# Performance work log

Hardware: AMD Instinct MI355X
Metric: run time of the kernel (lower is better)

The kernel has to match this reference:

```python
import jax, jax.numpy as jnp
import numpy as np

BETA = 0.1       # reputation weight
GAMMA = 0.1      # load penalty weight
EXPL_C = 0.1     # UCB exploration constant
LOAD_EMA = 0.9   # load EMA alpha
TOP_K = 2
EPS = 1e-10


def setup_inputs() -> dict:
    key = jax.random.key(0)
    k1, k2, k3, k4, k5 = jax.random.split(key, 5)
    B, S, H, E = 4, 4096, 2048, 64
    return {
        "x": jax.random.normal(k1, (B, S, H), dtype=jnp.float32),
        "gate_w": jax.random.normal(k2, (E, H), dtype=jnp.float32) * (1.0 / np.sqrt(H)),
        "reputation": jax.random.normal(k3, (E,), dtype=jnp.float32),
        "loads": jax.random.uniform(k4, (E,), dtype=jnp.float32),
        "counts": jax.random.uniform(k5, (E,), dtype=jnp.float32),
        "total_decisions": 1000000,
    }


def reference(x, gate_w, reputation, loads, counts, total_decisions):
    B, S, H = x.shape
    E = gate_w.shape[0]
    x_flat = x.reshape(-1, H)                                  # [T, H]
    base_logits = jnp.einsum("th,eh->te", x_flat, gate_w)      # [T, E]

    # current_batch_assignments is None -> current_loads = expert_loads
    updated_loads = LOAD_EMA * loads + (1.0 - LOAD_EMA) * loads  # [E]

    # UCB-style exploration bonus, broadcast over tokens
    expl = EXPL_C * jnp.sqrt(jnp.log(jnp.float32(total_decisions) + 1.0) / (counts + EPS))  # [E]

    selection_scores = (base_logits
                        + BETA * reputation[None, :]
                        - GAMMA * updated_loads[None, :]
                        + expl[None, :])                        # [T, E]

    top_k_scores, top_k_indices = jax.lax.top_k(selection_scores, TOP_K)  # [T, K]
    routing_weights = jax.nn.softmax(top_k_scores, axis=-1).reshape(B, S, TOP_K)
    expert_indices = top_k_indices.reshape(B, S, TOP_K)

    # differentiable load-balancing aux loss
    router_probs = jax.nn.softmax(selection_scores.astype(jnp.float32), axis=-1)  # [T, E]
    expert_gate = jax.nn.one_hot(top_k_indices, E, dtype=jnp.float32).sum(axis=1)  # [T, E]
    tokens_per_expert = expert_gate.mean(axis=0)               # [E]
    router_prob_per_expert = router_probs.mean(axis=0)         # [E]
    aux_loss = (tokens_per_expert * router_prob_per_expert).sum() * E

    return routing_weights, expert_indices, aux_loss
```

## Files before the change

kernel.cpp:

```cpp
#include <hip/hip_runtime.h>
#include <cmath>

#define HDIM 2048
#define H4   (HDIM / 4)
#define NEXP 64
#define TTOT 16384
#define KSPLIT 2
#define KBLK (HDIM / KSPLIT)
#define BKC  64
#define NCHUNK (KBLK / BKC)
#define BTOK 64
#define LDT  72
#define LDS_SC 65

#define WS_PARTIAL_OFF 128
#define PARTIAL_FLOATS ((size_t)(TTOT / BTOK) * KSPLIT * BTOK * NEXP)

typedef short  bf16x8 __attribute__((ext_vector_type(8)));
typedef float  f32x16 __attribute__((ext_vector_type(16)));

__device__ __forceinline__ unsigned bf_rn_u(float f, float* back) {
    unsigned u = __float_as_uint(f);
    unsigned r = (u + 0x7fffu + ((u >> 16) & 1u)) & 0xffff0000u;
    *back = __uint_as_float(r);
    return r;
}

__global__ __launch_bounds__(256, 2) void router_gemm_mfma(
    const float* __restrict__ x,
    const float* __restrict__ gw,
    float* __restrict__ partial,
    float* __restrict__ accs)
{
    __shared__ short aT[3][BTOK][LDT];
    __shared__ short bT[3][NEXP][LDT];

    const int tid  = threadIdx.x;
    const int lane = tid & 63;
    const int l31  = lane & 31;
    const int lhi  = lane >> 5;
    const int w    = tid >> 6;
    const int wm   = w & 1;
    const int wn   = w >> 1;
    const int tb   = blockIdx.x;
    const int kg   = blockIdx.y;
    const int T0   = tb * BTOK;

    if (tb == 0 && kg == 0 && tid < 2 * NEXP) accs[tid] = 0.0f;

    const int srow = tid >> 2;
    const int scol = tid & 3;

    const float4* __restrict__ x4 = reinterpret_cast<const float4*>(x)
        + (size_t)(T0 + srow) * H4 + (size_t)kg * (H4 / 2) + scol;
    const float4* __restrict__ g4 = reinterpret_cast<const float4*>(gw)
        + (size_t)srow * H4 + (size_t)kg * (H4 / 2) + scol;

    f32x16 acc;
    #pragma unroll
    for (int i = 0; i < 16; ++i) acc[i] = 0.0f;

    const short* aP[3];
    const short* bP[3];
    #pragma unroll
    for (int v = 0; v < 3; ++v) {
        aP[v] = &aT[v][32 * wm + l31][8 * lhi];
        bP[v] = &bT[v][32 * wn + l31][8 * lhi];
    }

    float4 xa[4], xb[4];

#define LOAD_CHUNK(CH) do {                                                    \
        _Pragma("unroll")                                                      \
        for (int j = 0; j < 4; ++j) {                                          \
            xa[j] = x4[(CH) * (BKC / 4) + 4 * j];                              \
            xb[j] = g4[(CH) * (BKC / 4) + 4 * j];                              \
        } } while (0)

#define SPLIT_STORE(TILE, ROW, FV, JJ) do {                                    \
        const float _f[4] = {(FV).x, (FV).y, (FV).z, (FV).w};                  \
        unsigned _h[4], _m[4], _l[4];                                          \
        _Pragma("unroll")                                                      \
        for (int u = 0; u < 4; ++u) {                                          \
            float _b0, _b1;                                                    \
            _h[u] = bf_rn_u(_f[u], &_b0);                                      \
            const float _r1 = _f[u] - _b0;                                     \
            _m[u] = bf_rn_u(_r1, &_b1);                                        \
            const float _r2 = _r1 - _b1;                                       \
            _l[u] = __float_as_uint(_r2) + 0x8000u;                            \
        }                                                                      \
        const int _kl = 4 * (scol + 4 * (JJ));                                 \
        *reinterpret_cast<uint2*>(&TILE[0][ROW][_kl]) =                        \
            make_uint2(__builtin_amdgcn_perm(_h[1], _h[0], 0x07060302u),       \
                       __builtin_amdgcn_perm(_h[3], _h[2], 0x07060302u));      \
        *reinterpret_cast<uint2*>(&TILE[1][ROW][_kl]) =                        \
            make_uint2(__builtin_amdgcn_perm(_m[1], _m[0], 0x07060302u),       \
                       __builtin_amdgcn_perm(_m[3], _m[2], 0x07060302u));      \
        *reinterpret_cast<uint2*>(&TILE[2][ROW][_kl]) =                        \
            make_uint2(__builtin_amdgcn_perm(_l[1], _l[0], 0x07060302u),       \
                       __builtin_amdgcn_perm(_l[3], _l[2], 0x07060302u));      \
    } while (0)

    LOAD_CHUNK(0);

    for (int ch = 0; ch < NCHUNK; ++ch) {
        #pragma unroll
        for (int j = 0; j < 4; ++j) {
            SPLIT_STORE(aT, srow, xa[j], j);
            SPLIT_STORE(bT, srow, xb[j], j);
        }
        __syncthreads();

        if (ch + 1 < NCHUNK) LOAD_CHUNK(ch + 1);

        #pragma unroll
        for (int ks = 0; ks < 4; ++ks) {
            bf16x8 ah = *reinterpret_cast<const bf16x8*>(aP[0] + 16 * ks);
            bf16x8 am = *reinterpret_cast<const bf16x8*>(aP[1] + 16 * ks);
            bf16x8 al = *reinterpret_cast<const bf16x8*>(aP[2] + 16 * ks);
            bf16x8 bh = *reinterpret_cast<const bf16x8*>(bP[0] + 16 * ks);
            bf16x8 bm = *reinterpret_cast<const bf16x8*>(bP[1] + 16 * ks);
            bf16x8 bl = *reinterpret_cast<const bf16x8*>(bP[2] + 16 * ks);
            acc = __builtin_amdgcn_mfma_f32_32x32x16_bf16(ah, bh, acc, 0, 0, 0);
            acc = __builtin_amdgcn_mfma_f32_32x32x16_bf16(ah, bm, acc, 0, 0, 0);
            acc = __builtin_amdgcn_mfma_f32_32x32x16_bf16(am, bh, acc, 0, 0, 0);
            acc = __builtin_amdgcn_mfma_f32_32x32x16_bf16(ah, bl, acc, 0, 0, 0);
            acc = __builtin_amdgcn_mfma_f32_32x32x16_bf16(am, bm, acc, 0, 0, 0);
            acc = __builtin_amdgcn_mfma_f32_32x32x16_bf16(al, bh, acc, 0, 0, 0);
        }
        __syncthreads();
    }
#undef LOAD_CHUNK
#undef SPLIT_STORE

    float* pbase = partial + ((size_t)tb * KSPLIT + kg) * (BTOK * NEXP);
    const int e = 32 * wn + l31;
    #pragma unroll
    for (int r = 0; r < 16; ++r) {
        const int t_loc = 32 * wm + (r & 3) + 8 * (r >> 2) + 4 * lhi;
        pbase[(size_t)t_loc * NEXP + e] = acc[r];
    }
}

__global__ __launch_bounds__(256) void router_reduce(
    const float* __restrict__ partial,
    const float* __restrict__ rep,
    const float* __restrict__ loads,
    const float* __restrict__ counts,
    const int*   __restrict__ total_dec,
    float* __restrict__ out_w,
    float* __restrict__ out_idx,
    float* __restrict__ prob_acc,
    float* __restrict__ gate_acc)
{
    __shared__ float sc_s[BTOK][LDS_SC];
    __shared__ float bias_s[NEXP];
    __shared__ float m_s[BTOK], zi_s[BTOK];
    __shared__ int   i1_s[BTOK], i2_s[BTOK];

    const int tid = threadIdx.x;
    const int rt  = blockIdx.x;
    const int t0  = rt * BTOK;

    if (tid < NEXP) {
        float L = logf((float)(*total_dec) + 1.0f);
        bias_s[tid] = 0.1f * rep[tid] - 0.1f * loads[tid]
                    + 0.1f * sqrtf(L / (counts[tid] + 1e-10f));
    }
    __syncthreads();

    const float* p = partial + (size_t)rt * KSPLIT * (BTOK * NEXP);
    #pragma unroll
    for (int o = 0; o < (BTOK * NEXP) / 256; ++o) {
        const int idx = o * 256 + tid;
        float s = p[idx] + p[BTOK * NEXP + idx];
        sc_s[idx >> 6][idx & 63] = s + bias_s[idx & 63];
    }
    __syncthreads();

    if (tid < BTOK) {
        const int t = tid;
        float m1 = -INFINITY, m2 = -INFINITY;
        int   i1 = 0, i2 = 0;
        for (int e = 0; e < NEXP; ++e) {
            const float s = sc_s[t][e];
            if (s > m1)      { m2 = m1; i2 = i1; m1 = s; i1 = e; }
            else if (s > m2) { m2 = s; i2 = e; }
        }
        float z = 0.0f;
        for (int e = 0; e < NEXP; ++e) z += __expf(sc_s[t][e] - m1);

        const float e2  = expf(m2 - m1);
        const float inv = 1.0f / (1.0f + e2);
        const int   gt  = t0 + t;
        reinterpret_cast<float2*>(out_w)[gt]   = make_float2(inv, e2 * inv);
        reinterpret_cast<float2*>(out_idx)[gt] = make_float2((float)i1, (float)i2);
        m_s[t] = m1; zi_s[t] = 1.0f / z; i1_s[t] = i1; i2_s[t] = i2;
    }
    __syncthreads();

    if (tid < NEXP) {
        const int e = tid;
        float ps = 0.0f, gs = 0.0f;
        for (int t = 0; t < BTOK; ++t) {
            ps += __expf(sc_s[t][e] - m_s[t]) * zi_s[t];
            gs += (float)((i1_s[t] == e) + (i2_s[t] == e));
        }
        atomicAdd(&prob_acc[e], ps);
        atomicAdd(&gate_acc[e], gs);
    }
}

#define BKF  32
#define LDAF (64 + 4)
__global__ __launch_bounds__(256) void router_main(
    const float* __restrict__ x,
    const float* __restrict__ gw,
    const float* __restrict__ rep,
    const float* __restrict__ loads,
    const float* __restrict__ counts,
    const int*   __restrict__ total_dec,
    float* __restrict__ out_w,
    float* __restrict__ out_idx,
    float* __restrict__ prob_acc,
    float* __restrict__ gate_acc)
{
    __shared__ float a_s[2][BKF][LDAF];
    __shared__ float b_s[2][BKF][LDAF];
    __shared__ float sc_s[64][LDS_SC];
    __shared__ float bias_s[NEXP];
    __shared__ float m_s[64], z_s[64];
    __shared__ int   i1_s[64], i2_s[64];

    const int tid = threadIdx.x;
    const int tx  = tid & 15;
    const int ty  = tid >> 4;
    const int r0  = tid >> 3;
    const int c4  = tid & 7;
    const int t0  = blockIdx.x * 64;

    if (tid < NEXP) {
        float L = logf((float)(*total_dec) + 1.0f);
        bias_s[tid] = 0.1f * rep[tid] - 0.1f * loads[tid]
                    + 0.1f * sqrtf(L / (counts[tid] + 1e-10f));
    }

    const float4* __restrict__ x4 = reinterpret_cast<const float4*>(x) + (size_t)t0 * H4;
    const float4* __restrict__ g4 = reinterpret_cast<const float4*>(gw);

    float acc[4][4] = {};

#define STORE_TILE(BUFI, A0, A1, B0, B1) do {                                  \
        float _t0[4] = {(A0).x, (A0).y, (A0).z, (A0).w};                       \
        float _t1[4] = {(A1).x, (A1).y, (A1).z, (A1).w};                       \
        float _t2[4] = {(B0).x, (B0).y, (B0).z, (B0).w};                       \
        float _t3[4] = {(B1).x, (B1).y, (B1).z, (B1).w};                       \
        _Pragma("unroll")                                                      \
        for (int u = 0; u < 4; ++u) {                                          \
            a_s[BUFI][c4 * 4 + u][r0]      = _t0[u];                           \
            a_s[BUFI][c4 * 4 + u][r0 + 32] = _t1[u];                           \
            b_s[BUFI][c4 * 4 + u][r0]      = _t2[u];                           \
            b_s[BUFI][c4 * 4 + u][r0 + 32] = _t3[u];                           \
        } } while (0)

    {
        float4 a0 = x4[(size_t)r0 * H4 + c4];
        float4 a1 = x4[(size_t)(r0 + 32) * H4 + c4];
        float4 b0 = g4[(size_t)r0 * H4 + c4];
        float4 b1 = g4[(size_t)(r0 + 32) * H4 + c4];
        STORE_TILE(0, a0, a1, b0, b1);
    }
    __syncthreads();

    int buf = 0;
    for (int it = 0; it < HDIM / BKF; ++it) {
        float4 na0, na1, nb0, nb1;
        const bool has_next = (it + 1 < HDIM / BKF);
        if (has_next) {
            const int k4 = (it + 1) * (BKF / 4);
            na0 = x4[(size_t)r0 * H4 + k4 + c4];
            na1 = x4[(size_t)(r0 + 32) * H4 + k4 + c4];
            nb0 = g4[(size_t)r0 * H4 + k4 + c4];
            nb1 = g4[(size_t)(r0 + 32) * H4 + k4 + c4];
        }
        #pragma unroll
        for (int kk = 0; kk < BKF; ++kk) {
            const float4 afv = *reinterpret_cast<const float4*>(&a_s[buf][kk][ty * 4]);
            const float4 bfv = *reinterpret_cast<const float4*>(&b_s[buf][kk][tx * 4]);
            const float af[4] = {afv.x, afv.y, afv.z, afv.w};
            const float bf[4] = {bfv.x, bfv.y, bfv.z, bfv.w};
            #pragma unroll
            for (int i = 0; i < 4; ++i)
                #pragma unroll
                for (int j = 0; j < 4; ++j)
                    acc[i][j] = fmaf(af[i], bf[j], acc[i][j]);
        }
        if (has_next) STORE_TILE(buf ^ 1, na0, na1, nb0, nb1);
        __syncthreads();
        buf ^= 1;
    }
#undef STORE_TILE

    #pragma unroll
    for (int i = 0; i < 4; ++i)
        #pragma unroll
        for (int j = 0; j < 4; ++j)
            sc_s[ty * 4 + i][tx * 4 + j] = acc[i][j] + bias_s[tx * 4 + j];
    __syncthreads();

    if (tid < 64) {
        const int t = tid;
        float m1 = -INFINITY, m2 = -INFINITY;
        int   i1 = 0, i2 = 0;
        for (int e = 0; e < NEXP; ++e) {
            const float s = sc_s[t][e];
            if (s > m1)      { m2 = m1; i2 = i1; m1 = s; i1 = e; }
            else if (s > m2) { m2 = s; i2 = e; }
        }
        float z = 0.0f;
        for (int e = 0; e < NEXP; ++e) z += expf(sc_s[t][e] - m1);
        const float e2  = expf(m2 - m1);
        const float inv = 1.0f / (1.0f + e2);
        const int   gt  = t0 + t;
        reinterpret_cast<float2*>(out_w)[gt]   = make_float2(inv, e2 * inv);
        reinterpret_cast<float2*>(out_idx)[gt] = make_float2((float)i1, (float)i2);
        m_s[t] = m1; z_s[t] = z; i1_s[t] = i1; i2_s[t] = i2;
    }
    __syncthreads();

    if (tid < NEXP) {
        const int e = tid;
        float ps = 0.0f, gs = 0.0f;
        for (int t = 0; t < 64; ++t) {
            ps += expf(sc_s[t][e] - m_s[t]) / z_s[t];
            gs += (float)((i1_s[t] == e) + (i2_s[t] == e));
        }
        atomicAdd(&prob_acc[e], ps);
        atomicAdd(&gate_acc[e], gs);
    }
}

__global__ void router_aux(const float* __restrict__ prob_acc,
                           const float* __restrict__ gate_acc,
                           float* __restrict__ out_aux)
{
    const float invT = 1.0f / (float)TTOT;
    const int e = threadIdx.x;
    float v = (gate_acc[e] * invT) * (prob_acc[e] * invT);
    #pragma unroll
    for (int off = 32; off > 0; off >>= 1)
        v += __shfl_down(v, off);
    if (e == 0) out_aux[0] = v * (float)NEXP;
}

extern "C" void kernel_launch(void* const* d_in, const int* in_sizes, int n_in,
                              void* d_out, int out_size, void* d_ws, size_t ws_size,
                              hipStream_t stream)
{
    const float* x      = (const float*)d_in[0];
    const float* gw     = (const float*)d_in[1];
    const float* rep    = (const float*)d_in[2];
    const float* loads  = (const float*)d_in[3];
    const float* counts = (const float*)d_in[4];
    const int*   total  = (const int*)d_in[5];

    float* out     = (float*)d_out;
    float* out_w   = out;
    float* out_idx = out + 32768;
    float* out_aux = out + 65536;

    float* prob_acc = (float*)d_ws;
    float* gate_acc = prob_acc + NEXP;
    float* partial  = (float*)d_ws + WS_PARTIAL_OFF;

    const size_t ws_needed = (WS_PARTIAL_OFF + PARTIAL_FLOATS) * sizeof(float);

    if (ws_size >= ws_needed) {
        router_gemm_mfma<<<dim3(TTOT / BTOK, KSPLIT), dim3(256), 0, stream>>>(
            x, gw, partial, prob_acc);
        router_reduce<<<dim3(TTOT / BTOK), dim3(256), 0, stream>>>(
            partial, rep, loads, counts, total, out_w, out_idx, prob_acc, gate_acc);
    } else {
        hipMemsetAsync(d_ws, 0, WS_PARTIAL_OFF * sizeof(float), stream);
        router_main<<<dim3(TTOT / 64), dim3(256), 0, stream>>>(
            x, gw, rep, loads, counts, total, out_w, out_idx, prob_acc, gate_acc);
    }
    router_aux<<<dim3(1), dim3(64), 0, stream>>>(prob_acc, gate_acc, out_aux);
}
```

Baseline: 228.9 us.

## Pre-split gate weights into bf16x3 once and stream them into the GEMM

Adds a small kernel that splits gate_w into three bf16 planes (hi/mid/lo) in workspace once per call, so the 256x2 GEMM blocks load the pre-split weights instead of each redoing the fp32 to bf16x3 split. The per-element split on both operands is also rewritten to use packed hardware bf16 conversion. This removes redundant VALU work on the weight tile in every block, at the cost of an extra launch and 768KB of extra workspace traffic. The low component is now rounded rather than truncated with a bias, which slightly changes numerics.

```diff
diff --git a/kernel.cpp b/kernel.cpp
--- a/kernel.cpp
+++ b/kernel.cpp
@@ -1,4 +1,5 @@
 #include <hip/hip_runtime.h>
+#include <hip/hip_bf16.h>
 #include <cmath>
 
 #define HDIM 2048
@@ -13,24 +14,55 @@
 #define LDT  72
 #define LDS_SC 65
 
-#define WS_PARTIAL_OFF 128
-#define PARTIAL_FLOATS ((size_t)(TTOT / BTOK) * KSPLIT * BTOK * NEXP)
-
+typedef unsigned short u16;
 typedef short  bf16x8 __attribute__((ext_vector_type(8)));
 typedef float  f32x16 __attribute__((ext_vector_type(16)));
 
-__device__ __forceinline__ unsigned bf_rn_u(float f, float* back) {
-    unsigned u = __float_as_uint(f);
-    unsigned r = (u + 0x7fffu + ((u >> 16) & 1u)) & 0xffff0000u;
-    *back = __uint_as_float(r);
+#define WS_GWS_OFF   128
+#define GWS_FLOATS   (3 * NEXP * HDIM / 2)
+#define WS_PARTIAL_OFF (WS_GWS_OFF + GWS_FLOATS)
+#define PARTIAL_FLOATS ((size_t)(TTOT / BTOK) * KSPLIT * BTOK * NEXP)
+#define ESTR (NEXP * HDIM)
+
+__device__ __forceinline__ unsigned cvtpk(float a, float b) {
+    __hip_bfloat162 h2 = __float22bfloat162_rn(make_float2(a, b));
+    unsigned r;
+    __builtin_memcpy(&r, &h2, sizeof(r));
     return r;
+}
+__device__ __forceinline__ void split3(float4 f, uint2* H, uint2* M, uint2* L) {
+    unsigned h0 = cvtpk(f.x, f.y), h1 = cvtpk(f.z, f.w);
+    float r0 = f.x - __uint_as_float(h0 << 16);
+    float r1 = f.y - __uint_as_float(h0 & 0xffff0000u);
+    float r2 = f.z - __uint_as_float(h1 << 16);
+    float r3 = f.w - __uint_as_float(h1 & 0xffff0000u);
+    unsigned m0 = cvtpk(r0, r1), m1 = cvtpk(r2, r3);
+    float s0 = r0 - __uint_as_float(m0 << 16);
+    float s1 = r1 - __uint_as_float(m0 & 0xffff0000u);
+    float s2 = r2 - __uint_as_float(m1 << 16);
+    float s3 = r3 - __uint_as_float(m1 & 0xffff0000u);
+    unsigned l0 = cvtpk(s0, s1), l1 = cvtpk(s2, s3);
+    *H = make_uint2(h0, h1); *M = make_uint2(m0, m1); *L = make_uint2(l0, l1);
+}
+
+__global__ __launch_bounds__(256) void split_gw_k(
+    const float* __restrict__ gw, u16* __restrict__ gws,
+    float* __restrict__ accs)
+{
+    const int i = blockIdx.x * 256 + threadIdx.x;
+    if (blockIdx.x == 0 && threadIdx.x < 2 * NEXP) accs[threadIdx.x] = 0.0f;
+    float4 f = reinterpret_cast<const float4*>(gw)[i];
+    uint2 h, m, l;
+    split3(f, &h, &m, &l);
+    reinterpret_cast<uint2*>(gws)[i]            = h;
+    reinterpret_cast<uint2*>(gws + ESTR)[i]     = m;
+    reinterpret_cast<uint2*>(gws + 2 * ESTR)[i] = l;
 }
 
 __global__ __launch_bounds__(256, 2) void router_gemm_mfma(
     const float* __restrict__ x,
-    const float* __restrict__ gw,
-    float* __restrict__ partial,
-    float* __restrict__ accs)
+    const u16*   __restrict__ gws,
+    float* __restrict__ partial)
 {
     __shared__ short aT[3][BTOK][LDT];
     __shared__ short bT[3][NEXP][LDT];
@@ -46,15 +78,12 @@
     const int kg   = blockIdx.y;
     const int T0   = tb * BTOK;
 
-    if (tb == 0 && kg == 0 && tid < 2 * NEXP) accs[tid] = 0.0f;
-
     const int srow = tid >> 2;
     const int scol = tid & 3;
 
     const float4* __restrict__ x4 = reinterpret_cast<const float4*>(x)
         + (size_t)(T0 + srow) * H4 + (size_t)kg * (H4 / 2) + scol;
-    const float4* __restrict__ g4 = reinterpret_cast<const float4*>(gw)
-        + (size_t)srow * H4 + (size_t)kg * (H4 / 2) + scol;
+    const u16* __restrict__ gwsB = gws + (size_t)srow * HDIM + kg * KBLK + scol * 16;
 
     f32x16 acc;
     #pragma unroll
@@ -68,46 +97,37 @@
         bP[v] = &bT[v][32 * wn + l31][8 * lhi];
     }
 
-    float4 xa[4], xb[4];
+    float4 xa[4];
 
 #define LOAD_CHUNK(CH) do {                                                    \
         _Pragma("unroll")                                                      \
-        for (int j = 0; j < 4; ++j) {                                          \
+        for (int j = 0; j < 4; ++j)                                            \
             xa[j] = x4[(CH) * (BKC / 4) + 4 * j];                              \
-            xb[j] = g4[(CH) * (BKC / 4) + 4 * j];                              \
-        } } while (0)
-
-#define SPLIT_STORE(TILE, ROW, FV, JJ) do {                                    \
-        const float _f[4] = {(FV).x, (FV).y, (FV).z, (FV).w};                  \
-        unsigned _h[4], _m[4], _l[4];                                          \
-        _Pragma("unroll")                                                      \
-        for (int u = 0; u < 4; ++u) {                                          \
-            float _b0, _b1;                                                    \
-            _h[u] = bf_rn_u(_f[u], &_b0);                                      \
-            const float _r1 = _f[u] - _b0;                                     \
-            _m[u] = bf_rn_u(_r1, &_b1);                                        \
-            const float _r2 = _r1 - _b1;                                       \
-            _l[u] = __float_as_uint(_r2) + 0x8000u;                            \
-        }                                                                      \
-        const int _kl = 4 * (scol + 4 * (JJ));                                 \
-        *reinterpret_cast<uint2*>(&TILE[0][ROW][_kl]) =                        \
-            make_uint2(__builtin_amdgcn_perm(_h[1], _h[0], 0x07060302u),       \
-                       __builtin_amdgcn_perm(_h[3], _h[2], 0x07060302u));      \
-        *reinterpret_cast<uint2*>(&TILE[1][ROW][_kl]) =                        \
-            make_uint2(__builtin_amdgcn_perm(_m[1], _m[0], 0x07060302u),       \
-                       __builtin_amdgcn_perm(_m[3], _m[2], 0x07060302u));      \
-        *reinterpret_cast<uint2*>(&TILE[2][ROW][_kl]) =                        \
-            make_uint2(__builtin_amdgcn_perm(_l[1], _l[0], 0x07060302u),       \
-                       __builtin_amdgcn_perm(_l[3], _l[2], 0x07060302u));      \
     } while (0)
 
     LOAD_CHUNK(0);
 
     for (int ch = 0; ch < NCHUNK; ++ch) {
+        uint4 bq[3][2];
+        #pragma unroll
+        for (int v = 0; v < 3; ++v) {
+            const u16* p = gwsB + (size_t)v * ESTR + ch * 64;
+            bq[v][0] = *reinterpret_cast<const uint4*>(p);
+            bq[v][1] = *reinterpret_cast<const uint4*>(p + 8);
+        }
         #pragma unroll
         for (int j = 0; j < 4; ++j) {
-            SPLIT_STORE(aT, srow, xa[j], j);
-            SPLIT_STORE(bT, srow, xb[j], j);
+            uint2 h, m, l;
+            split3(xa[j], &h, &m, &l);
+            const int kl = 4 * (scol + 4 * j);
+            *reinterpret_cast<uint2*>(&aT[0][srow][kl]) = h;
+            *reinterpret_cast<uint2*>(&aT[1][srow][kl]) = m;
+            *reinterpret_cast<uint2*>(&aT[2][srow][kl]) = l;
+        }
+        #pragma unroll
+        for (int v = 0; v < 3; ++v) {
+            *reinterpret_cast<uint4*>(&bT[v][srow][scol * 16])     = bq[v][0];
+            *reinterpret_cast<uint4*>(&bT[v][srow][scol * 16 + 8]) = bq[v][1];
         }
         __syncthreads();
 
@@ -131,7 +151,6 @@
         __syncthreads();
     }
 #undef LOAD_CHUNK
-#undef SPLIT_STORE
 
     float* pbase = partial + ((size_t)tb * KSPLIT + kg) * (BTOK * NEXP);
     const int e = 32 * wn + l31;
@@ -371,17 +390,20 @@
 
     float* prob_acc = (float*)d_ws;
     float* gate_acc = prob_acc + NEXP;
+    u16*   gws      = (u16*)((float*)d_ws + WS_GWS_OFF);
     float* partial  = (float*)d_ws + WS_PARTIAL_OFF;
 
     const size_t ws_needed = (WS_PARTIAL_OFF + PARTIAL_FLOATS) * sizeof(float);
 
     if (ws_size >= ws_needed) {
+        split_gw_k<<<dim3(NEXP * HDIM / 4 / 256), dim3(256), 0, stream>>>(
+            gw, gws, prob_acc);
         router_gemm_mfma<<<dim3(TTOT / BTOK, KSPLIT), dim3(256), 0, stream>>>(
-            x, gw, partial, prob_acc);
+            x, gws, partial);
         router_reduce<<<dim3(TTOT / BTOK), dim3(256), 0, stream>>>(
             partial, rep, loads, counts, total, out_w, out_idx, prob_acc, gate_acc);
     } else {
-        hipMemsetAsync(d_ws, 0, WS_PARTIAL_OFF * sizeof(float), stream);
+        (void)hipMemsetAsync(d_ws, 0, 2 * NEXP * sizeof(float), stream);
         router_main<<<dim3(TTOT / 64), dim3(256), 0, stream>>>(
             x, gw, rep, loads, counts, total, out_w, out_idx, prob_acc, gate_acc);
     }
```

After: 231.9 us. Within noise of the previous version (+1.3%).
